# Performance work log

Hardware: AMD Instinct MI355X
Metric: run time of the kernel (lower is better)

The kernel has to match this reference:

```python
import jax, jax.numpy as jnp
import numpy as np

HIDDEN = 1024
SEQ = 32768


def setup_inputs() -> dict:
    key = jax.random.key(0)
    k1, k2, k3, k4 = jax.random.split(key, 4)
    scale = 1.0 / np.sqrt(HIDDEN)
    return {
        "hidden": jax.random.normal(k1, (HIDDEN,), dtype=jnp.float32),
        "encoder_outputs": jax.random.normal(k2, (SEQ, HIDDEN), dtype=jnp.float32),
        "W": jax.random.normal(k3, (HIDDEN, HIDDEN), dtype=jnp.float32) * scale,
        "b": jax.random.normal(k4, (HIDDEN,), dtype=jnp.float32) * scale,
    }


def reference(hidden, encoder_outputs, W, b):
    # method == 'general': energy_i = Linear(enc_i); score_i = hidden . energy_i
    # Batched: energies = (enc @ W.T + b) @ hidden   -> [S]
    proj = jnp.einsum("sh,oh->so", encoder_outputs, W) + b  # [S, H]
    energies = proj @ hidden                                  # [S]
    attn = jax.nn.softmax(energies, axis=-1)                  # softmax over seq
    return attn[None, None, :]                                # [1, 1, S]
```

## Files before the change

kernel.cpp:

```cpp
#include <hip/hip_runtime.h>
#include <math.h>

#define H 1024
#define S 32768

__global__ void matvec_partial_kernel(const float* __restrict__ W,
                                      const float* __restrict__ hidden,
                                      float* __restrict__ vpart) {
    const int t = threadIdx.x;
    const int b = blockIdx.x;
    const int h4 = t * 4;
    float4 acc = make_float4(0.f, 0.f, 0.f, 0.f);
    const int o0 = b * 16;
#pragma unroll
    for (int i = 0; i < 16; ++i) {
        const int o = o0 + i;
        const float hv = hidden[o];
        const float4 w = *reinterpret_cast<const float4*>(&W[(size_t)o * H + h4]);
        acc.x += hv * w.x;
        acc.y += hv * w.y;
        acc.z += hv * w.z;
        acc.w += hv * w.w;
    }
    *reinterpret_cast<float4*>(&vpart[(size_t)b * H + h4]) = acc;
}

__global__ void matvec_reduce_kernel(const float* __restrict__ vpart,
                                     float* __restrict__ v) {
    const int t = threadIdx.x;
    const int h4 = t * 4;
    float4 acc = make_float4(0.f, 0.f, 0.f, 0.f);
#pragma unroll 8
    for (int b = 0; b < 64; ++b) {
        const float4 p = *reinterpret_cast<const float4*>(&vpart[(size_t)b * H + h4]);
        acc.x += p.x;
        acc.y += p.y;
        acc.z += p.z;
        acc.w += p.w;
    }
    *reinterpret_cast<float4*>(&v[h4]) = acc;
}

__global__ void energies_kernel(const float* __restrict__ enc,
                                const float* __restrict__ v,
                                float* __restrict__ energies,
                                float* __restrict__ mpart,
                                float* __restrict__ spart) {
    const int wave = threadIdx.x >> 6;
    const int lane = threadIdx.x & 63;
    const int gwave = blockIdx.x * 4 + wave;
    const int s0 = gwave * 4;

    float4 vv[4];
#pragma unroll
    for (int j = 0; j < 4; ++j)
        vv[j] = *reinterpret_cast<const float4*>(&v[j * 256 + lane * 4]);

    float e[4];
#pragma unroll
    for (int r = 0; r < 4; ++r) {
        const float* row = enc + (size_t)(s0 + r) * H;
        float acc = 0.f;
#pragma unroll
        for (int j = 0; j < 4; ++j) {
            const float4 ev = *reinterpret_cast<const float4*>(&row[j * 256 + lane * 4]);
            acc += ev.x * vv[j].x + ev.y * vv[j].y + ev.z * vv[j].z + ev.w * vv[j].w;
        }
#pragma unroll
        for (int off = 32; off > 0; off >>= 1)
            acc += __shfl_xor(acc, off, 64);
        e[r] = acc;
    }

    if (lane == 0) {
        energies[s0 + 0] = e[0];
        energies[s0 + 1] = e[1];
        energies[s0 + 2] = e[2];
        energies[s0 + 3] = e[3];
    }

    const float mw = fmaxf(fmaxf(e[0], e[1]), fmaxf(e[2], e[3]));
    const float sw = __expf(e[0] - mw) + __expf(e[1] - mw) +
                     __expf(e[2] - mw) + __expf(e[3] - mw);

    __shared__ float lm[4], ls[4];
    if (lane == 0) { lm[wave] = mw; ls[wave] = sw; }
    __syncthreads();
    if (threadIdx.x == 0) {
        const float m = fmaxf(fmaxf(lm[0], lm[1]), fmaxf(lm[2], lm[3]));
        const float s = ls[0] * __expf(lm[0] - m) + ls[1] * __expf(lm[1] - m) +
                        ls[2] * __expf(lm[2] - m) + ls[3] * __expf(lm[3] - m);
        mpart[blockIdx.x] = m;
        spart[blockIdx.x] = s;
    }
}

__global__ void finalize_kernel(const float* __restrict__ energies,
                                const float* __restrict__ mpart,
                                const float* __restrict__ spart,
                                float* __restrict__ out) {
    __shared__ float red[16];
    __shared__ float gm_s, gs_s;
    const int t = threadIdx.x;
    const int lane = t & 63;
    const int wid = t >> 6;

    float m = fmaxf(mpart[t], mpart[t + 1024]);
#pragma unroll
    for (int off = 32; off > 0; off >>= 1)
        m = fmaxf(m, __shfl_xor(m, off, 64));
    if (lane == 0) red[wid] = m;
    __syncthreads();
    if (t == 0) {
        float mm = red[0];
#pragma unroll
        for (int i = 1; i < 16; ++i) mm = fmaxf(mm, red[i]);
        gm_s = mm;
    }
    __syncthreads();
    const float gm = gm_s;

    float s = spart[t] * __expf(mpart[t] - gm) +
              spart[t + 1024] * __expf(mpart[t + 1024] - gm);
#pragma unroll
    for (int off = 32; off > 0; off >>= 1)
        s += __shfl_xor(s, off, 64);
    __syncthreads();
    if (lane == 0) red[wid] = s;
    __syncthreads();
    if (t == 0) {
        float ss = 0.f;
#pragma unroll
        for (int i = 0; i < 16; ++i) ss += red[i];
        gs_s = ss;
    }
    __syncthreads();
    const float inv = 1.0f / gs_s;

#pragma unroll
    for (int k = 0; k < S / 1024; ++k)
        out[t + k * 1024] = __expf(energies[t + k * 1024] - gm) * inv;
}

extern "C" void kernel_launch(void* const* d_in, const int* in_sizes, int n_in,
                              void* d_out, int out_size, void* d_ws, size_t ws_size,
                              hipStream_t stream) {
    const float* hidden = (const float*)d_in[0];
    const float* enc    = (const float*)d_in[1];
    const float* W      = (const float*)d_in[2];
    float* out = (float*)d_out;

    float* vpart    = (float*)d_ws;
    float* v        = vpart + 64 * H;
    float* energies = v + H;
    float* mpart    = energies + S;
    float* spart    = mpart + 2048;

    matvec_partial_kernel<<<64, 256, 0, stream>>>(W, hidden, vpart);
    matvec_reduce_kernel<<<1, 256, 0, stream>>>(vpart, v);
    energies_kernel<<<2048, 256, 0, stream>>>(enc, v, energies, mpart, spart);
    finalize_kernel<<<1, 1024, 0, stream>>>(energies, mpart, spart, out);
}
```

Baseline: 211.4 us.

## Fuse attention pipeline into one cooperative kernel with grid-wide syncs

Replaces the four separate launches (partial matvec, reduce, energies, finalize) with a single cooperative kernel that uses grid.sync between phases. Energies stay in registers, so the intermediate energies array is never written or re-read, and the softmax normalisation is done by every block. The W·hidden matvec is spread over 256 blocks and the reduction over 8 blocks, in place of 64 blocks and 1 block. In exchange it needs all 2048 blocks co-resident and pays for three grid barriers, and every block re-reads the partial max/sum arrays. The old multi-kernel path is kept as a fallback if the cooperative launch fails.

```diff
diff --git a/kernel.cpp b/kernel.cpp
--- a/kernel.cpp
+++ b/kernel.cpp
@@ -1,8 +1,128 @@
 #include <hip/hip_runtime.h>
+#include <hip/hip_cooperative_groups.h>
 #include <math.h>
+
+namespace cg = cooperative_groups;
 
 #define H 1024
 #define S 32768
+#define GRID 2048
+#define TPB 256
+
+extern "C" __global__ void __launch_bounds__(TPB, 8)
+attn_fused_kernel(const float* __restrict__ W,
+                  const float* __restrict__ hidden,
+                  const float* __restrict__ enc,
+                  float* __restrict__ vpart,
+                  float* __restrict__ v,
+                  float* __restrict__ mpart,
+                  float* __restrict__ spart,
+                  float* __restrict__ out)
+{
+    cg::grid_group grid = cg::this_grid();
+    const int t    = threadIdx.x;
+    const int b    = blockIdx.x;
+    const int wave = t >> 6;
+    const int lane = t & 63;
+    const int s0   = (b * 4 + wave) * 4;
+
+    __shared__ float lm[4], ls[4];
+    __shared__ float rm[4], rs[4];
+
+    if (b < 256) {
+        const int h4 = t * 4;
+        const int o0 = b * 4;
+        float4 acc = make_float4(0.f, 0.f, 0.f, 0.f);
+#pragma unroll
+        for (int i = 0; i < 4; ++i) {
+            const float  hv = hidden[o0 + i];
+            const float4 w  = *reinterpret_cast<const float4*>(&W[(size_t)(o0 + i) * H + h4]);
+            acc.x += hv * w.x; acc.y += hv * w.y;
+            acc.z += hv * w.z; acc.w += hv * w.w;
+        }
+        *reinterpret_cast<float4*>(&vpart[(size_t)b * H + h4]) = acc;
+    }
+    grid.sync();
+
+    if (b < 8 && t < 128) {
+        const int c = b * 128 + t;
+        float acc = 0.f;
+#pragma unroll 16
+        for (int p = 0; p < 256; ++p)
+            acc += vpart[(size_t)p * H + c];
+        v[c] = acc;
+    }
+    grid.sync();
+
+    float4 vv[4];
+#pragma unroll
+    for (int j = 0; j < 4; ++j)
+        vv[j] = *reinterpret_cast<const float4*>(&v[j * 256 + lane * 4]);
+
+    float e[4];
+#pragma unroll
+    for (int r = 0; r < 4; ++r) {
+        const float* row = enc + (size_t)(s0 + r) * H;
+        float acc = 0.f;
+#pragma unroll
+        for (int j = 0; j < 4; ++j) {
+            const float4 ev = *reinterpret_cast<const float4*>(&row[j * 256 + lane * 4]);
+            acc += ev.x * vv[j].x + ev.y * vv[j].y + ev.z * vv[j].z + ev.w * vv[j].w;
+        }
+#pragma unroll
+        for (int off = 32; off > 0; off >>= 1)
+            acc += __shfl_xor(acc, off, 64);
+        e[r] = acc;
+    }
+
+    const float mw = fmaxf(fmaxf(e[0], e[1]), fmaxf(e[2], e[3]));
+    const float sw = __expf(e[0] - mw) + __expf(e[1] - mw) +
+                     __expf(e[2] - mw) + __expf(e[3] - mw);
+    if (lane == 0) { lm[wave] = mw; ls[wave] = sw; }
+    __syncthreads();
+    if (t == 0) {
+        const float m = fmaxf(fmaxf(lm[0], lm[1]), fmaxf(lm[2], lm[3]));
+        const float s = ls[0] * __expf(lm[0] - m) + ls[1] * __expf(lm[1] - m) +
+                        ls[2] * __expf(lm[2] - m) + ls[3] * __expf(lm[3] - m);
+        mpart[b] = m; spart[b] = s;
+    }
+    grid.sync();
+
+    float m8[8], s8[8];
+#pragma unroll
+    for (int i = 0; i < 8; ++i) {
+        m8[i] = mpart[t * 8 + i];
+        s8[i] = spart[t * 8 + i];
+    }
+    float mt = m8[0];
+#pragma unroll
+    for (int i = 1; i < 8; ++i) mt = fmaxf(mt, m8[i]);
+#pragma unroll
+    for (int off = 32; off > 0; off >>= 1)
+        mt = fmaxf(mt, __shfl_xor(mt, off, 64));
+    if (lane == 0) rm[wave] = mt;
+    __syncthreads();
+    const float gm = fmaxf(fmaxf(rm[0], rm[1]), fmaxf(rm[2], rm[3]));
+
+    float st = 0.f;
+#pragma unroll
+    for (int i = 0; i < 8; ++i) st += s8[i] * __expf(m8[i] - gm);
+#pragma unroll
+    for (int off = 32; off > 0; off >>= 1)
+        st += __shfl_xor(st, off, 64);
+    if (lane == 0) rs[wave] = st;
+    __syncthreads();
+    const float inv = 1.0f / (rs[0] + rs[1] + rs[2] + rs[3]);
+
+    if (lane == 0) {
+        float4 o4;
+        o4.x = __expf(e[0] - gm) * inv;
+        o4.y = __expf(e[1] - gm) * inv;
+        o4.z = __expf(e[2] - gm) * inv;
+        o4.w = __expf(e[3] - gm) * inv;
+        *reinterpret_cast<float4*>(&out[s0]) = o4;
+    }
+}
 
 __global__ void matvec_partial_kernel(const float* __restrict__ W,
                                       const float* __restrict__ hidden,
@@ -17,10 +137,8 @@
         const int o = o0 + i;
         const float hv = hidden[o];
         const float4 w = *reinterpret_cast<const float4*>(&W[(size_t)o * H + h4]);
-        acc.x += hv * w.x;
-        acc.y += hv * w.y;
-        acc.z += hv * w.z;
-        acc.w += hv * w.w;
+        acc.x += hv * w.x; acc.y += hv * w.y;
+        acc.z += hv * w.z; acc.w += hv * w.w;
     }
     *reinterpret_cast<float4*>(&vpart[(size_t)b * H + h4]) = acc;
 }
@@ -33,10 +151,7 @@
 #pragma unroll 8
     for (int b = 0; b < 64; ++b) {
         const float4 p = *reinterpret_cast<const float4*>(&vpart[(size_t)b * H + h4]);
-        acc.x += p.x;
-        acc.y += p.y;
-        acc.z += p.z;
-        acc.w += p.w;
+        acc.x += p.x; acc.y += p.y; acc.z += p.z; acc.w += p.w;
     }
     *reinterpret_cast<float4*>(&v[h4]) = acc;
 }
@@ -150,14 +265,28 @@
     const float* W      = (const float*)d_in[2];
     float* out = (float*)d_out;
 
-    float* vpart    = (float*)d_ws;
-    float* v        = vpart + 64 * H;
-    float* energies = v + H;
-    float* mpart    = energies + S;
-    float* spart    = mpart + 2048;
-
-    matvec_partial_kernel<<<64, 256, 0, stream>>>(W, hidden, vpart);
-    matvec_reduce_kernel<<<1, 256, 0, stream>>>(vpart, v);
-    energies_kernel<<<2048, 256, 0, stream>>>(enc, v, energies, mpart, spart);
-    finalize_kernel<<<1, 1024, 0, stream>>>(energies, mpart, spart, out);
-}
+    float* vpart = (float*)d_ws;
+    float* v     = vpart + 256 * H;
+    float* mpart = v + H;
+    float* spart = mpart + GRID;
+
+    void* args[] = { (void*)&W, (void*)&hidden, (void*)&enc,
+                     (void*)&vpart, (void*)&v, (void*)&mpart, (void*)&spart,
+                     (void*)&out };
+
+    hipError_t err = hipLaunchCooperativeKernel(
+        reinterpret_cast<void*>(attn_fused_kernel),
+        dim3(GRID), dim3(TPB), args, 0, stream);
+
+    if (err != hipSuccess) {
+        float* fvpart    = (float*)d_ws;
+        float* fv        = fvpart + 64 * H;
+        float* fenergies = fv + H;
+        float* fmpart    = fenergies + S;
+        float* fspart    = fmpart + 2048;
+        matvec_partial_kernel<<<64, 256, 0, stream>>>(W, hidden, fvpart);
+        matvec_reduce_kernel<<<1, 256, 0, stream>>>(fvpart, fv);
+        energies_kernel<<<2048, 256, 0, stream>>>(enc, fv, fenergies, fmpart, fspart);
+        finalize_kernel<<<1, 1024, 0, stream>>>(fenergies, fmpart, fspart, out);
+    }
+}
```

Result: slower. 747.4 us (+253.6%).

## Parallelize softmax finalize across blocks and rebalance matvec split

Applied to the files above, without the earlier changes.

The finalize step moves from a single 1024-thread block to 128 blocks. Each block redundantly reduces the 2048 partial max/sum values, then normalizes its own slice of outputs. The W·hidden matvec now uses 256 partial blocks of 4 rows each, and its reduction runs in 4 blocks of 64 threads over 256 partials. The aim is to remove the serial single-block tail stages, at the cost of redundant partial reductions and a larger, longer partial-sum reduction.

```diff
diff --git a/kernel.cpp b/kernel.cpp
--- a/kernel.cpp
+++ b/kernel.cpp
@@ -10,33 +10,27 @@
     const int t = threadIdx.x;
     const int b = blockIdx.x;
     const int h4 = t * 4;
+    const int o0 = b * 4;
     float4 acc = make_float4(0.f, 0.f, 0.f, 0.f);
-    const int o0 = b * 16;
 #pragma unroll
-    for (int i = 0; i < 16; ++i) {
-        const int o = o0 + i;
-        const float hv = hidden[o];
-        const float4 w = *reinterpret_cast<const float4*>(&W[(size_t)o * H + h4]);
-        acc.x += hv * w.x;
-        acc.y += hv * w.y;
-        acc.z += hv * w.z;
-        acc.w += hv * w.w;
+    for (int i = 0; i < 4; ++i) {
+        const float  hv = hidden[o0 + i];
+        const float4 w  = *reinterpret_cast<const float4*>(&W[(size_t)(o0 + i) * H + h4]);
+        acc.x += hv * w.x; acc.y += hv * w.y;
+        acc.z += hv * w.z; acc.w += hv * w.w;
     }
     *reinterpret_cast<float4*>(&vpart[(size_t)b * H + h4]) = acc;
 }
 
 __global__ void matvec_reduce_kernel(const float* __restrict__ vpart,
                                      float* __restrict__ v) {
-    const int t = threadIdx.x;
-    const int h4 = t * 4;
+    const int idx = blockIdx.x * 64 + threadIdx.x;
+    const int h4 = idx * 4;
     float4 acc = make_float4(0.f, 0.f, 0.f, 0.f);
 #pragma unroll 8
-    for (int b = 0; b < 64; ++b) {
-        const float4 p = *reinterpret_cast<const float4*>(&vpart[(size_t)b * H + h4]);
-        acc.x += p.x;
-        acc.y += p.y;
-        acc.z += p.z;
-        acc.w += p.w;
+    for (int p = 0; p < 256; ++p) {
+        const float4 q = *reinterpret_cast<const float4*>(&vpart[(size_t)p * H + h4]);
+        acc.x += q.x; acc.y += q.y; acc.z += q.z; acc.w += q.w;
     }
     *reinterpret_cast<float4*>(&v[h4]) = acc;
 }
@@ -99,47 +93,38 @@
                                 const float* __restrict__ mpart,
                                 const float* __restrict__ spart,
                                 float* __restrict__ out) {
-    __shared__ float red[16];
-    __shared__ float gm_s, gs_s;
     const int t = threadIdx.x;
     const int lane = t & 63;
-    const int wid = t >> 6;
+    const int wave = t >> 6;
+    __shared__ float rm[4], rs[4];
 
-    float m = fmaxf(mpart[t], mpart[t + 1024]);
+    const float4 ma = *reinterpret_cast<const float4*>(&mpart[t * 8]);
+    const float4 mb = *reinterpret_cast<const float4*>(&mpart[t * 8 + 4]);
+    const float4 sa = *reinterpret_cast<const float4*>(&spart[t * 8]);
+    const float4 sb = *reinterpret_cast<const float4*>(&spart[t * 8 + 4]);
+
+    float mt = fmaxf(fmaxf(fmaxf(ma.x, ma.y), fmaxf(ma.z, ma.w)),
+                     fmaxf(fmaxf(mb.x, mb.y), fmaxf(mb.z, mb.w)));
 #pragma unroll
     for (int off = 32; off > 0; off >>= 1)
-        m = fmaxf(m, __shfl_xor(m, off, 64));
-    if (lane == 0) red[wid] = m;
+        mt = fmaxf(mt, __shfl_xor(mt, off, 64));
+    if (lane == 0) rm[wave] = mt;
     __syncthreads();
-    if (t == 0) {
-        float mm = red[0];
-#pragma unroll
-        for (int i = 1; i < 16; ++i) mm = fmaxf(mm, red[i]);
-        gm_s = mm;
-    }
-    __syncthreads();
-    const float gm = gm_s;
+    const float gm = fmaxf(fmaxf(rm[0], rm[1]), fmaxf(rm[2], rm[3]));
 
-    float s = spart[t] * __expf(mpart[t] - gm) +
-              spart[t + 1024] * __expf(mpart[t + 1024] - gm);
+    float st = sa.x * __expf(ma.x - gm) + sa.y * __expf(ma.y - gm) +
+               sa.z * __expf(ma.z - gm) + sa.w * __expf(ma.w - gm) +
+               sb.x * __expf(mb.x - gm) + sb.y * __expf(mb.y - gm) +
+               sb.z * __expf(mb.z - gm) + sb.w * __expf(mb.w - gm);
 #pragma unroll
     for (int off = 32; off > 0; off >>= 1)
-        s += __shfl_xor(s, off, 64);
+        st += __shfl_xor(st, off, 64);
+    if (lane == 0) rs[wave] = st;
     __syncthreads();
-    if (lane == 0) red[wid] = s;
-    __syncthreads();
-    if (t == 0) {
-        float ss = 0.f;
-#pragma unroll
-        for (int i = 0; i < 16; ++i) ss += red[i];
-        gs_s = ss;
-    }
-    __syncthreads();
-    const float inv = 1.0f / gs_s;
+    const float inv = 1.0f / (rs[0] + rs[1] + rs[2] + rs[3]);
 
-#pragma unroll
-    for (int k = 0; k < S / 1024; ++k)
-        out[t + k * 1024] = __expf(energies[t + k * 1024] - gm) * inv;
+    const int i = blockIdx.x * 256 + t;
+    out[i] = __expf(energies[i] - gm) * inv;
 }
 
 extern "C" void kernel_launch(void* const* d_in, const int* in_sizes, int n_in,
@@ -151,13 +136,13 @@
     float* out = (float*)d_out;
 
     float* vpart    = (float*)d_ws;
-    float* v        = vpart + 64 * H;
+    float* v        = vpart + 256 * H;
     float* energies = v + H;
     float* mpart    = energies + S;
     float* spart    = mpart + 2048;
 
-    matvec_partial_kernel<<<64, 256, 0, stream>>>(W, hidden, vpart);
-    matvec_reduce_kernel<<<1, 256, 0, stream>>>(vpart, v);
+    matvec_partial_kernel<<<256, 256, 0, stream>>>(W, hidden, vpart);
+    matvec_reduce_kernel<<<4, 64, 0, stream>>>(vpart, v);
     energies_kernel<<<2048, 256, 0, stream>>>(enc, v, energies, mpart, spart);
-    finalize_kernel<<<1, 1024, 0, stream>>>(energies, mpart, spart, out);
+    finalize_kernel<<<128, 256, 0, stream>>>(energies, mpart, spart, out);
 }
```

New measurement: 218.5 us. 3.4% more time.
